# Optimization experiments

Hardware: AMD Instinct MI355X
Metric: run time of the kernel (lower is better)

## Reference

```python
import jax, jax.numpy as jnp
import numpy as np

LATENT = 100
INIT_SIZE = 8   # img_size // 4
NUM = 200       # LIF time steps
BETA = 0.95
THR = 1.0
CH_OUT = 3

# snntorch ATan surrogate spike (alpha=2 -> grad = 1/(1+(pi*u)^2))
@jax.custom_vjp
def spike_fn(x):
    return (x > 0).astype(x.dtype)

def _spike_fwd(x):
    return (x > 0).astype(x.dtype), x

def _spike_bwd(x, g):
    return (g / (1.0 + (jnp.pi * x) ** 2),)

spike_fn.defvjp(_spike_fwd, _spike_bwd)

def batchnorm(x, gamma, beta, eps):
    # training-mode BN: batch statistics over (N,H,W), biased variance (as torch)
    mean = x.mean(axis=(0, 2, 3), keepdims=True)
    var = ((x - mean) ** 2).mean(axis=(0, 2, 3), keepdims=True)
    xh = (x - mean) * jax.lax.rsqrt(var + eps)
    return xh * gamma[None, :, None, None] + beta[None, :, None, None]

def upsample2x(x):  # nearest-neighbor, scale 2
    return jnp.repeat(jnp.repeat(x, 2, axis=2), 2, axis=3)

def conv2d(x, w, b):  # 3x3, stride 1, padding 1
    y = jax.lax.conv_general_dilated(x, w, (1, 1), [(1, 1), (1, 1)],
                                     dimension_numbers=("NCHW", "OIHW", "NCHW"))
    return y + b[None, :, None, None]

def leaky_relu(x):
    return jnp.where(x >= 0, x, 0.2 * x)

def setup_inputs() -> dict:
    key = jax.random.key(0)
    ks = jax.random.split(key, 8)
    B = 8
    def n(k, shape, s=0.02):
        return jax.random.normal(k, shape, dtype=jnp.float32) * s
    return {
        "z": jax.random.normal(ks[0], (B, LATENT), dtype=jnp.float32),
        "w_l1": n(ks[1], (LATENT, 128 * INIT_SIZE ** 2)),
        "b_l1": jnp.zeros((128 * INIT_SIZE ** 2,), jnp.float32),
        "g1": jnp.ones((128,), jnp.float32), "be1": jnp.zeros((128,), jnp.float32),
        "w_c1": n(ks[2], (128, NUM * 128, 3, 3), 0.005),
        "b_c1": jnp.zeros((128,), jnp.float32),
        "g2": jnp.ones((128,), jnp.float32), "be2": jnp.zeros((128,), jnp.float32),
        "w_c2": n(ks[3], (64, 128, 3, 3)),
        "b_c2": jnp.zeros((64,), jnp.float32),
        "g3": jnp.ones((64,), jnp.float32), "be3": jnp.zeros((64,), jnp.float32),
        "w_c3": n(ks[4], (CH_OUT, 64, 3, 3)),
        "b_c3": jnp.zeros((CH_OUT,), jnp.float32),
    }

def reference(z, w_l1, b_l1, g1, be1, w_c1, b_c1, g2, be2, w_c2, b_c2, g3, be3, w_c3, b_c3):
    B = z.shape[0]
    out = z @ w_l1 + b_l1                       # (B, 128*8*8)
    out = out.reshape(B, 128, INIT_SIZE, INIT_SIZE)
    out = batchnorm(out, g1, be1, 1e-5)
    out = upsample2x(out)                       # (B,128,16,16) constant LIF input

    def lif_step(mem, _):
        # snntorch Leaky, reset-by-subtraction; reset detached from grad
        reset = jax.lax.stop_gradient((mem > THR).astype(mem.dtype))
        mem = BETA * mem + out - reset * THR
        spk = spike_fn(mem - THR)
        return mem, spk

    mem0 = jnp.zeros_like(out)
    _, spk_rec = jax.lax.scan(lif_step, mem0, None, length=NUM)  # (NUM,B,128,16,16)
    # faithful to torch.stack(dim=0).reshape(B, -1, 16, 16)
    x = spk_rec.reshape(B, NUM * 128, 16, 16)
    x = conv2d(x, w_c1, b_c1)                   # (B,128,16,16)
    x = leaky_relu(batchnorm(x, g2, be2, 0.8))  # BatchNorm2d(128, 0.8): eps=0.8
    x = upsample2x(x)                           # (B,128,32,32)
    x = conv2d(x, w_c2, b_c2)                   # (B,64,32,32)
    x = leaky_relu(batchnorm(x, g3, be3, 0.8))
    x = conv2d(x, w_c3, b_c3)                   # (B,3,32,32)
    return jnp.tanh(x)
```

## Files before the change

kernel.cpp:

```cpp
#include <hip/hip_runtime.h>
#include <math.h>


#define WROW 25632
#define SROW 25664

typedef _Float16 half8 __attribute__((ext_vector_type(8)));
typedef float f32x4 __attribute__((ext_vector_type(4)));
typedef unsigned int uint4v __attribute__((ext_vector_type(4)));

union AFrag { uint4v u4; unsigned int u[4]; half8 h; };

__global__ __launch_bounds__(256) void k_lin_bn1(
    const float* __restrict__ z, const float* __restrict__ w,
    const float* __restrict__ bias, const float* __restrict__ g1,
    const float* __restrict__ be1, float* __restrict__ I) {
  int ch = blockIdx.x, tid = threadIdx.x;
  __shared__ float red[256];
  int hw = tid & 63, b0 = tid >> 6;
  int j = ch * 64 + hw;
  float acc0 = bias[j], acc1 = acc0;
  const float* zp0 = z + b0 * 100;
  const float* zp1 = z + (b0 + 4) * 100;
  for (int l = 0; l < 100; ++l) {
    float wv = w[l * 8192 + j];
    acc0 += zp0[l] * wv;
    acc1 += zp1[l] * wv;
  }
  float v0 = acc0, v1 = acc1;
  red[tid] = v0 + v1; __syncthreads();
  for (int s = 128; s > 0; s >>= 1) { if (tid < s) red[tid] += red[tid + s]; __syncthreads(); }
  float mean = red[0] * (1.0f / 512.0f);
  __syncthreads();
  float d0 = v0 - mean, d1 = v1 - mean;
  red[tid] = d0 * d0 + d1 * d1; __syncthreads();
  for (int s = 128; s > 0; s >>= 1) { if (tid < s) red[tid] += red[tid + s]; __syncthreads(); }
  float var = red[0] * (1.0f / 512.0f);
  float coef = g1[ch] / sqrtf(var + 1e-5f);
  float beta = be1[ch];
  float q0 = (v0 - mean) * coef + beta;
  float q1 = (v1 - mean) * coef + beta;
#pragma unroll
  for (int k = 0; k < 2; ++k) {
    int n = k ? (tid + 256) : tid; float q = k ? q1 : q0;
    int b = n >> 6, hh = n & 63, h = hh >> 3, ww = hh & 7;
    float* o = I + (size_t)(b * 128 + ch) * 256 + (2 * h) * 16 + 2 * ww;
    o[0] = q; o[1] = q; o[16] = q; o[17] = q;
  }
}

__global__ __launch_bounds__(256) void k_lif(
    const float* __restrict__ I, unsigned char* __restrict__ spkTb) {
  int g = blockIdx.x * 256 + threadIdx.x;
  int px = g >> 10, plane = g & 1023;
  int lane = threadIdx.x & 63;
  float in = I[plane * 256 + px];
  int pos = ((px >> 4) + 1) * 18 + (px & 15) + 1;
  unsigned long long* wsrow =
      (unsigned long long*)(spkTb + (size_t)pos * SROW + ((plane - lane) >> 3));
  float mem = 0.0f;
  for (int t = 0; t < 200; ++t) {
    float reset = (mem > 1.0f) ? 1.0f : 0.0f;
    mem = 0.95f * mem + in - reset;
    unsigned long long m = __ballot(mem > 1.0f);
    if (lane == 0) wsrow[t * 16] = m;
  }
}

__global__ __launch_bounds__(256) void k_wtrans(
    const float* __restrict__ wc1, _Float16* __restrict__ wT) {
  __shared__ float t[2304];
  int oc = blockIdx.x / 100, cg = blockIdx.x % 100;
  int c0 = cg * 256, tid = threadIdx.x;
  const float* src = wc1 + (size_t)oc * 230400 + (size_t)c0 * 9;
#pragma unroll
  for (int i = 0; i < 9; ++i) t[tid + i * 256] = src[tid + i * 256];
  __syncthreads();
#pragma unroll
  for (int tap = 0; tap < 9; ++tap)
    wT[(size_t)(tap * 128 + oc) * WROW + c0 + tid] = (_Float16)t[tid * 9 + tap];
}

__device__ inline void expandp(unsigned int b, AFrag& f) {
  unsigned int lo = ((b & 0xFu) * 0x00204081u) & 0x01010101u;
  unsigned int hi = ((b >> 4) * 0x00204081u) & 0x01010101u;
  lo *= 0x3Cu; hi *= 0x3Cu;
  f.u[0] = __builtin_amdgcn_perm(0u, lo, 0x01040004u);
  f.u[1] = __builtin_amdgcn_perm(0u, lo, 0x03040204u);
  f.u[2] = __builtin_amdgcn_perm(0u, hi, 0x01040004u);
  f.u[3] = __builtin_amdgcn_perm(0u, hi, 0x03040204u);
}

__device__ __forceinline__ void gll16(const void* g, void* l) {
  __builtin_amdgcn_global_load_lds(
      (const __attribute__((address_space(1))) unsigned int*)g,
      (__attribute__((address_space(3))) unsigned int*)l, 16, 0, 0);
}

__global__ __launch_bounds__(256, 2) void k_conv1_mfma(
    const unsigned char* __restrict__ spkTb, const _Float16* __restrict__ wT,
    _Float16* __restrict__ y1p) {
  int v = (blockIdx.x & 7) * 50 + (blockIdx.x >> 3);
  int tl = v >> 3;
  int r = v & 7;
  int half = r >> 2, bp = r & 3;
  int b0 = bp * 2;
  int tid = threadIdx.x;
  int wave = tid >> 6, lane = tid & 63;
  int quad = lane >> 4, l16 = lane & 15;
  int qs = quad * 8;
  int h0 = wave * 4;

  __shared__ _Float16 As[2][8192];

  int ocl = tid >> 4;
  int sc0 = (tid & 15) ^ ocl;
  const char* srcA0 = (const char*)wT + (size_t)tl * 1024
                    + (size_t)(half * 64 + ocl) * (WROW * 2) + sc0 * 16;

  const unsigned char* rowp[8];
#pragma unroll
  for (int nt = 0; nt < 8; ++nt)
    rowp[nt] = spkTb + (b0 + (nt >> 2)) * 3200 + tl * 64
             + (size_t)((h0 + (nt & 3)) * 18 + l16) * SROW;

  int dsb[4];
#pragma unroll
  for (int s = 0; s < 4; ++s)
    dsb[s] = l16 * 256 + ((s * 64 + quad * 16) ^ (l16 << 4));

  f32x4 acc[4][8] = {};

#pragma unroll
  for (int i = 0; i < 4; ++i)
    gll16(srcA0 + (size_t)i * (16 * WROW * 2), (char*)As + i * 4096 + wave * 1024);
  __syncthreads();

#pragma unroll 2
  for (int bs = 0; bs < 36; ++bs) {
    int tap = bs >> 2, s128 = bs & 3;
    int dh = tap / 3, dw = tap - dh * 3;
    uint4v bx[8];
    int boff = (dh * 18 + dw) * SROW + s128 * 16;
#pragma unroll
    for (int nt = 0; nt < 8; ++nt)
      bx[nt] = *(const uint4v*)(rowp[nt] + boff);
    if (bs + 1 < 36) {
      int tapn = (bs + 1) >> 2, s128n = (bs + 1) & 3;
      size_t aoff = (size_t)tapn * ((size_t)128 * WROW * 2) + (size_t)s128n * 256;
      char* dst = (char*)As + ((bs + 1) & 1) * 16384 + wave * 1024;
#pragma unroll
      for (int i = 0; i < 4; ++i)
        gll16(srcA0 + (size_t)i * (16 * WROW * 2) + aoff, dst + i * 4096);
    }
    const char* cA = (const char*)As + (bs & 1) * 16384;
#pragma unroll
    for (int s = 0; s < 4; ++s) {
      AFrag a[4];
#pragma unroll
      for (int mt = 0; mt < 4; ++mt)
        a[mt].u4 = *(const uint4v*)(cA + dsb[s] + mt * 4096);
#pragma unroll
      for (int nt = 0; nt < 8; ++nt) {
        AFrag bf; expandp((bx[nt][s] >> qs) & 0xFFu, bf);
#pragma unroll
        for (int mt = 0; mt < 4; ++mt)
          acc[mt][nt] = __builtin_amdgcn_mfma_f32_16x16x32_f16(
              a[mt].h, bf.h, acc[mt][nt], 0, 0, 0);
      }
    }
    __syncthreads();
  }

#pragma unroll
  for (int mt = 0; mt < 4; ++mt)
#pragma unroll
    for (int nt = 0; nt < 8; ++nt) {
      int bb = nt >> 2;
      int px = (h0 + (nt & 3)) * 16 + l16;
      _Float16* ob = y1p + (size_t)(tl * 8 + b0 + bb) * 32768 + half * 16384;
#pragma unroll
      for (int rr = 0; rr < 4; ++rr) {
        int oc = mt * 16 + quad * 4 + rr;
        ob[(size_t)oc * 256 + px] = (_Float16)acc[mt][nt][rr];
      }
    }
}

__global__ __launch_bounds__(256) void k_bn2_up(
    const _Float16* __restrict__ y1p, const float* __restrict__ bc1,
    const float* __restrict__ g2, const float* __restrict__ be2,
    float* __restrict__ x2p) {
  int ch = blockIdx.x, tid = threadIdx.x;
  __shared__ float red[256];

  for (int e = tid; e < 1056; e += 256) {
    int b = e / 132, i = e - b * 132;
    int rr, cc;
    if (i < 34)       { rr = 0;       cc = i; }
    else if (i < 68)  { rr = 33;      cc = i - 34; }
    else if (i < 100) { rr = i - 67;  cc = 0; }
    else              { rr = i - 99;  cc = 33; }
    x2p[(size_t)(b * 128 + ch) * 1156 + rr * 34 + cc] = 0.0f;
  }

  int pp = tid & 127;
  int bh = tid >> 7;
  float bias = bc1[ch];
  float a[4][2] = {};
  const char* base = (const char*)y1p + ((size_t)ch * 256 + pp * 2) * 2
                   + (size_t)bh * 4 * 65536;
  for (int tl = 0; tl < 50; ++tl) {
    const char* q = base + (size_t)tl * 524288;
#pragma unroll
    for (int k = 0; k < 4; ++k) {
      union { unsigned int u; _Float16 h[2]; } cv;
      cv.u = *(const unsigned int*)(q + (size_t)k * 65536);
      a[k][0] += (float)cv.h[0];
      a[k][1] += (float)cv.h[1];
    }
  }
  float vv[4][2]; float s = 0.0f;
#pragma unroll
  for (int k = 0; k < 4; ++k)
#pragma unroll
    for (int e = 0; e < 2; ++e) { vv[k][e] = a[k][e] + bias; s += vv[k][e]; }

  red[tid] = s; __syncthreads();
  for (int st = 128; st > 0; st >>= 1) { if (tid < st) red[tid] += red[tid + st]; __syncthreads(); }
  float mean = red[0] * (1.0f / 2048.0f);
  __syncthreads();
  s = 0.0f;
#pragma unroll
  for (int k = 0; k < 4; ++k)
#pragma unroll
    for (int e = 0; e < 2; ++e) { float d = vv[k][e] - mean; s += d * d; }
  red[tid] = s; __syncthreads();
  for (int st = 128; st > 0; st >>= 1) { if (tid < st) red[tid] += red[tid + st]; __syncthreads(); }
  float var = red[0] * (1.0f / 2048.0f);
  float coef = g2[ch] / sqrtf(var + 0.8f);
  float beta = be2[ch];
#pragma unroll
  for (int k = 0; k < 4; ++k)
#pragma unroll
    for (int e = 0; e < 2; ++e) {
      int b = bh * 4 + k, px = pp * 2 + e, h = px >> 4, w = px & 15;
      float q = (vv[k][e] - mean) * coef + beta;
      q = (q >= 0.0f) ? q : 0.2f * q;
      float* o = x2p + (size_t)(b * 128 + ch) * 1156 + (2 * h + 1) * 34 + (2 * w + 1);
      o[0] = q; o[1] = q; o[34] = q; o[35] = q;
    }
}

__global__ __launch_bounds__(256) void k_conv2(
    const float* __restrict__ x2p, const float* __restrict__ wc2,
    const float* __restrict__ bc2, float* __restrict__ y2) {
  int octile = blockIdx.x, b = blockIdx.y, pq = blockIdx.z;
  int tid = threadIdx.x;
  int p = pq * 256 + tid, h = p >> 5, w = p & 31;
  float a0 = 0.0f, a1 = 0.0f, a2 = 0.0f, a3 = 0.0f;
  const float* base = x2p + (size_t)(b * 128) * 1156 + h * 34 + w;
  const float* wb = wc2 + (size_t)(octile * 4) * 128 * 9;
  for (int ch = 0; ch < 128; ++ch) {
    const float* pp = base + (size_t)ch * 1156;
    float s0 = pp[0],  s1 = pp[1],  s2 = pp[2];
    float s3 = pp[34], s4 = pp[35], s5 = pp[36];
    float s6 = pp[68], s7 = pp[69], s8 = pp[70];
    const float* w0 = wb + (size_t)ch * 9;
    const float* w1 = wb + (size_t)(128 + ch) * 9;
    const float* w2 = wb + (size_t)(256 + ch) * 9;
    const float* w3 = wb + (size_t)(384 + ch) * 9;
    a0 += s0*w0[0]+s1*w0[1]+s2*w0[2]+s3*w0[3]+s4*w0[4]+s5*w0[5]+s6*w0[6]+s7*w0[7]+s8*w0[8];
    a1 += s0*w1[0]+s1*w1[1]+s2*w1[2]+s3*w1[3]+s4*w1[4]+s5*w1[5]+s6*w1[6]+s7*w1[7]+s8*w1[8];
    a2 += s0*w2[0]+s1*w2[1]+s2*w2[2]+s3*w2[3]+s4*w2[4]+s5*w2[5]+s6*w2[6]+s7*w2[7]+s8*w2[8];
    a3 += s0*w3[0]+s1*w3[1]+s2*w3[2]+s3*w3[3]+s4*w3[4]+s5*w3[5]+s6*w3[6]+s7*w3[7]+s8*w3[8];
  }
  int oc0 = octile * 4;
  y2[(size_t)(b * 64 + oc0 + 0) * 1024 + p] = a0 + bc2[oc0 + 0];
  y2[(size_t)(b * 64 + oc0 + 1) * 1024 + p] = a1 + bc2[oc0 + 1];
  y2[(size_t)(b * 64 + oc0 + 2) * 1024 + p] = a2 + bc2[oc0 + 2];
  y2[(size_t)(b * 64 + oc0 + 3) * 1024 + p] = a3 + bc2[oc0 + 3];
}

__global__ __launch_bounds__(256) void k_bn3(
    const float* __restrict__ y2, const float* __restrict__ g3,
    const float* __restrict__ be3, float* __restrict__ y2n) {
  int ch = blockIdx.x, tid = threadIdx.x;
  __shared__ float red[256];

  for (int e = tid; e < 1056; e += 256) {
    int b = e / 132, i = e - b * 132;
    int rr, cc;
    if (i < 34)       { rr = 0;       cc = i; }
    else if (i < 68)  { rr = 33;      cc = i - 34; }
    else if (i < 100) { rr = i - 67;  cc = 0; }
    else              { rr = i - 99;  cc = 33; }
    y2n[(size_t)(b * 64 + ch) * 1156 + rr * 34 + cc] = 0.0f;
  }

  float v[32]; float s = 0.0f;
#pragma unroll
  for (int k = 0; k < 32; ++k) {
    int n = tid + k * 256;
    v[k] = y2[(size_t)((n >> 10) * 64 + ch) * 1024 + (n & 1023)];
    s += v[k];
  }
  red[tid] = s; __syncthreads();
  for (int st = 128; st > 0; st >>= 1) { if (tid < st) red[tid] += red[tid + st]; __syncthreads(); }
  float mean = red[0] * (1.0f / 8192.0f);
  __syncthreads();
  s = 0.0f;
#pragma unroll
  for (int k = 0; k < 32; ++k) { float d = v[k] - mean; s += d * d; }
  red[tid] = s; __syncthreads();
  for (int st = 128; st > 0; st >>= 1) { if (tid < st) red[tid] += red[tid + st]; __syncthreads(); }
  float var = red[0] * (1.0f / 8192.0f);
  float coef = g3[ch] / sqrtf(var + 0.8f);
  float beta = be3[ch];
#pragma unroll
  for (int k = 0; k < 32; ++k) {
    int n = tid + k * 256;
    int b = n >> 10, px = n & 1023, h = px >> 5, w = px & 31;
    float q = (v[k] - mean) * coef + beta;
    q = (q >= 0.0f) ? q : 0.2f * q;
    y2n[(size_t)(b * 64 + ch) * 1156 + (h + 1) * 34 + (w + 1)] = q;
  }
}

__global__ __launch_bounds__(256) void k_conv3(
    const float* __restrict__ y2n, const float* __restrict__ wc3,
    const float* __restrict__ bc3, float* __restrict__ out) {
  int b = blockIdx.x >> 4, pg = blockIdx.x & 15;
  int tid = threadIdx.x;
  int pxl = tid & 63, cg = tid >> 6;
  int p = pg * 64 + pxl, h = p >> 5, w = p & 31;
  float a0 = 0.0f, a1 = 0.0f, a2 = 0.0f;
  const float* base = y2n + (size_t)(b * 64 + cg * 16) * 1156 + h * 34 + w;
  for (int c = 0; c < 16; ++c) {
    int ch = cg * 16 + c;
    const float* pp = base + (size_t)c * 1156;
    float s0 = pp[0],  s1 = pp[1],  s2 = pp[2];
    float s3 = pp[34], s4 = pp[35], s5 = pp[36];
    float s6 = pp[68], s7 = pp[69], s8 = pp[70];
    const float* w0 = wc3 + (size_t)ch * 9;
    const float* w1 = wc3 + (size_t)(64 + ch) * 9;
    const float* w2 = wc3 + (size_t)(128 + ch) * 9;
    a0 += s0*w0[0]+s1*w0[1]+s2*w0[2]+s3*w0[3]+s4*w0[4]+s5*w0[5]+s6*w0[6]+s7*w0[7]+s8*w0[8];
    a1 += s0*w1[0]+s1*w1[1]+s2*w1[2]+s3*w1[3]+s4*w1[4]+s5*w1[5]+s6*w1[6]+s7*w1[7]+s8*w1[8];
    a2 += s0*w2[0]+s1*w2[1]+s2*w2[2]+s3*w2[3]+s4*w2[4]+s5*w2[5]+s6*w2[6]+s7*w2[7]+s8*w2[8];
  }
  __shared__ float red[3][256];
  red[0][tid] = a0; red[1][tid] = a1; red[2][tid] = a2;
  __syncthreads();
  if (tid < 192) {
    int oc = tid >> 6, px = tid & 63;
    float sres = red[oc][px] + red[oc][px + 64] + red[oc][px + 128] + red[oc][px + 192];
    out[(size_t)(b * 3 + oc) * 1024 + pg * 64 + px] = tanhf(sres + bc3[oc]);
  }
}

extern "C" void kernel_launch(void* const* d_in, const int* in_sizes, int n_in,
                              void* d_out, int out_size, void* d_ws, size_t ws_size,
                              hipStream_t stream) {
  const float* z    = (const float*)d_in[0];
  const float* w_l1 = (const float*)d_in[1];
  const float* b_l1 = (const float*)d_in[2];
  const float* g1   = (const float*)d_in[3];
  const float* be1  = (const float*)d_in[4];
  const float* w_c1 = (const float*)d_in[5];
  const float* b_c1 = (const float*)d_in[6];
  const float* g2   = (const float*)d_in[7];
  const float* be2  = (const float*)d_in[8];
  const float* w_c2 = (const float*)d_in[9];
  const float* b_c2 = (const float*)d_in[10];
  const float* g3   = (const float*)d_in[11];
  const float* be3  = (const float*)d_in[12];
  const float* w_c3 = (const float*)d_in[13];
  const float* b_c3 = (const float*)d_in[14];
  float* out = (float*)d_out;

  char* ws = (char*)d_ws;
  _Float16* wT = (_Float16*)ws;
  unsigned char* spkTb = (unsigned char*)(ws + 59056128);
  float* I   = (float*)(ws + 67633408);
  _Float16* y1p = (_Float16*)(ws + 69730560);
  float* x2p = (float*)ws;
  float* y2n = (float*)(ws + 4734976);
  float* y2  = (float*)(ws + 7102464);

  size_t spkTb_bytes = (size_t)324 * SROW;

  hipMemsetAsync(spkTb, 0, spkTb_bytes, stream);

  k_wtrans <<<12800, 256, 0, stream>>>(w_c1, wT);
  k_lin_bn1<<<128, 256, 0, stream>>>(z, w_l1, b_l1, g1, be1, I);
  k_lif    <<<1024, 256, 0, stream>>>(I, spkTb);
  k_conv1_mfma<<<400, 256, 0, stream>>>(spkTb, wT, y1p);

  k_bn2_up <<<128, 256, 0, stream>>>(y1p, b_c1, g2, be2, x2p);
  k_conv2  <<<dim3(16, 8, 4), 256, 0, stream>>>(x2p, w_c2, b_c2, y2);
  k_bn3    <<<64, 256, 0, stream>>>(y2, g3, be3, y2n);
  k_conv3  <<<128, 256, 0, stream>>>(y2n, w_c3, b_c3, out);
}
```

Baseline: 457.4 us.

## Repartition conv1 split-K into 48 slices with one batch per block

The big conv1 MFMA kernel now splits the 200*128 channel reduction into 48 uneven slices of 4-5 chunks, with each block handling one batch image instead of two. This raises the block count from 400 to 768 and halves the accumulator tile, which allows three blocks per CU. The aim is better load balance and occupancy across the GPU's CUs. In exchange, each weight tile loaded into LDS is reused by only one batch image instead of two, and the loop now has a runtime trip count instead of a fixed unrolled one. The BN2 reduction is adjusted to sum 48 partial slices.

After: 437.0 us. 1.05x faster.

```diff
diff --git a/kernel.cpp b/kernel.cpp
--- a/kernel.cpp
+++ b/kernel.cpp
@@ -97,63 +97,66 @@
       (__attribute__((address_space(3))) unsigned int*)l, 16, 0, 0);
 }
 
-__global__ __launch_bounds__(256, 2) void k_conv1_mfma(
+__global__ __launch_bounds__(256, 3) void k_conv1_mfma(
     const unsigned char* __restrict__ spkTb, const _Float16* __restrict__ wT,
     _Float16* __restrict__ y1p) {
-  int v = (blockIdx.x & 7) * 50 + (blockIdx.x >> 3);
-  int tl = v >> 3;
-  int r = v & 7;
-  int half = r >> 2, bp = r & 3;
-  int b0 = bp * 2;
+  int v = (blockIdx.x & 7) * 96 + (blockIdx.x >> 3);
+  int sl = v >> 4;
+  int r = v & 15;
+  int half = r >> 3, b = r & 7;
   int tid = threadIdx.x;
   int wave = tid >> 6, lane = tid & 63;
   int quad = lane >> 4, l16 = lane & 15;
   int qs = quad * 8;
   int h0 = wave * 4;
 
+  int q0 = (sl * 25) / 6;
+  int qc = ((sl + 1) * 25) / 6 - q0;
+  int NBS = 9 * qc;
+
   __shared__ _Float16 As[2][8192];
 
   int ocl = tid >> 4;
   int sc0 = (tid & 15) ^ ocl;
-  const char* srcA0 = (const char*)wT + (size_t)tl * 1024
+  const char* srcA0 = (const char*)wT + (size_t)q0 * 256
                     + (size_t)(half * 64 + ocl) * (WROW * 2) + sc0 * 16;
 
-  const unsigned char* rowp[8];
-#pragma unroll
-  for (int nt = 0; nt < 8; ++nt)
-    rowp[nt] = spkTb + (b0 + (nt >> 2)) * 3200 + tl * 64
-             + (size_t)((h0 + (nt & 3)) * 18 + l16) * SROW;
+  const unsigned char* rowp[4];
+#pragma unroll
+  for (int nt = 0; nt < 4; ++nt)
+    rowp[nt] = spkTb + b * 3200 + q0 * 16
+             + (size_t)((h0 + nt) * 18 + l16) * SROW;
 
   int dsb[4];
 #pragma unroll
   for (int s = 0; s < 4; ++s)
     dsb[s] = l16 * 256 + ((s * 64 + quad * 16) ^ (l16 << 4));
 
-  f32x4 acc[4][8] = {};
+  f32x4 acc[4][4] = {};
 
 #pragma unroll
   for (int i = 0; i < 4; ++i)
     gll16(srcA0 + (size_t)i * (16 * WROW * 2), (char*)As + i * 4096 + wave * 1024);
   __syncthreads();
 
-#pragma unroll 2
-  for (int bs = 0; bs < 36; ++bs) {
-    int tap = bs >> 2, s128 = bs & 3;
+  int tap = 0, qi = 0;
+  for (int k = 0; k < NBS; ++k) {
     int dh = tap / 3, dw = tap - dh * 3;
-    uint4v bx[8];
-    int boff = (dh * 18 + dw) * SROW + s128 * 16;
-#pragma unroll
-    for (int nt = 0; nt < 8; ++nt)
+    uint4v bx[4];
+    int boff = (dh * 18 + dw) * SROW + qi * 16;
+#pragma unroll
+    for (int nt = 0; nt < 4; ++nt)
       bx[nt] = *(const uint4v*)(rowp[nt] + boff);
-    if (bs + 1 < 36) {
-      int tapn = (bs + 1) >> 2, s128n = (bs + 1) & 3;
-      size_t aoff = (size_t)tapn * ((size_t)128 * WROW * 2) + (size_t)s128n * 256;
-      char* dst = (char*)As + ((bs + 1) & 1) * 16384 + wave * 1024;
+    int qin = qi + 1, tapn = tap;
+    if (qin == qc) { qin = 0; tapn = tap + 1; }
+    if (k + 1 < NBS) {
+      size_t aoff = (size_t)tapn * ((size_t)128 * WROW * 2) + (size_t)qin * 256;
+      char* dst = (char*)As + ((k + 1) & 1) * 16384 + wave * 1024;
 #pragma unroll
       for (int i = 0; i < 4; ++i)
         gll16(srcA0 + (size_t)i * (16 * WROW * 2) + aoff, dst + i * 4096);
     }
-    const char* cA = (const char*)As + (bs & 1) * 16384;
+    const char* cA = (const char*)As + (k & 1) * 16384;
 #pragma unroll
     for (int s = 0; s < 4; ++s) {
       AFrag a[4];
@@ -161,7 +164,7 @@
       for (int mt = 0; mt < 4; ++mt)
         a[mt].u4 = *(const uint4v*)(cA + dsb[s] + mt * 4096);
 #pragma unroll
-      for (int nt = 0; nt < 8; ++nt) {
+      for (int nt = 0; nt < 4; ++nt) {
         AFrag bf; expandp((bx[nt][s] >> qs) & 0xFFu, bf);
 #pragma unroll
         for (int mt = 0; mt < 4; ++mt)
@@ -170,15 +173,15 @@
       }
     }
     __syncthreads();
-  }
-
+    tap = tapn; qi = qin;
+  }
+
+  _Float16* ob = y1p + (size_t)(sl * 8 + b) * 32768 + half * 16384;
 #pragma unroll
   for (int mt = 0; mt < 4; ++mt)
 #pragma unroll
-    for (int nt = 0; nt < 8; ++nt) {
-      int bb = nt >> 2;
-      int px = (h0 + (nt & 3)) * 16 + l16;
-      _Float16* ob = y1p + (size_t)(tl * 8 + b0 + bb) * 32768 + half * 16384;
+    for (int nt = 0; nt < 4; ++nt) {
+      int px = (h0 + nt) * 16 + l16;
 #pragma unroll
       for (int rr = 0; rr < 4; ++rr) {
         int oc = mt * 16 + quad * 4 + rr;
@@ -210,7 +213,7 @@
   float a[4][2] = {};
   const char* base = (const char*)y1p + ((size_t)ch * 256 + pp * 2) * 2
                    + (size_t)bh * 4 * 65536;
-  for (int tl = 0; tl < 50; ++tl) {
+  for (int tl = 0; tl < 48; ++tl) {
     const char* q = base + (size_t)tl * 524288;
 #pragma unroll
     for (int k = 0; k < 4; ++k) {
@@ -395,7 +398,7 @@
   k_wtrans <<<12800, 256, 0, stream>>>(w_c1, wT);
   k_lin_bn1<<<128, 256, 0, stream>>>(z, w_l1, b_l1, g1, be1, I);
   k_lif    <<<1024, 256, 0, stream>>>(I, spkTb);
-  k_conv1_mfma<<<400, 256, 0, stream>>>(spkTb, wT, y1p);
+  k_conv1_mfma<<<768, 256, 0, stream>>>(spkTb, wT, y1p);
 
   k_bn2_up <<<128, 256, 0, stream>>>(y1p, b_c1, g2, be2, x2p);
   k_conv2  <<<dim3(16, 8, 4), 256, 0, stream>>>(x2p, w_c2, b_c2, y2);
```
